# Kernel tuning notes

Measured on AMD Instinct MI355X. Metric: run time of the kernel, lower is better.

## Reference

```python
import jax, jax.numpy as jnp
import numpy as np

N = 100000   # nodes
E = 3200000  # edges
NC = 32


def cheb_conv(x, row, col, W, b):
    """PyG ChebConv with sym normalization and default lambda_max=2.
    Scaled Laplacian L_hat = 2L/lambda_max - I has zero diagonal and
    off-diagonal weights -d_i^{-1/2} d_j^{-1/2} (self-loops removed first).
    W: [K, in, out], b: [out] or None.
    """
    n = x.shape[0]
    ew = jnp.where(row != col, 1.0, 0.0).astype(x.dtype)  # remove_self_loops
    deg = jax.ops.segment_sum(ew, row, num_segments=n)
    dinv = jnp.where(deg > 0, jax.lax.rsqrt(jnp.maximum(deg, 1e-12)), 0.0)
    w = -ew * dinv[row] * dinv[col]  # [E] edge weights of L_hat

    def L(v):  # L_hat @ v via gather + segment-sum scatter
        return jax.ops.segment_sum(w[:, None] * v[col], row, num_segments=n)

    K = W.shape[0]
    Tx0 = x
    out = Tx0 @ W[0]
    if K > 1:
        Tx1 = L(x)
        out = out + Tx1 @ W[1]
        for k in range(2, K):  # Chebyshev recurrence T_k = 2 L T_{k-1} - T_{k-2}
            Tx2 = 2.0 * L(Tx1) - Tx0
            out = out + Tx2 @ W[k]
            Tx0, Tx1 = Tx1, Tx2
    if b is not None:
        out = out + b
    return out


def setup_inputs() -> dict:
    key = jax.random.key(0)
    ks = jax.random.split(key, 10)
    x = jax.random.normal(ks[0], (N, 3), dtype=jnp.float32)
    edge_index = jax.random.randint(ks[1], (2, E), 0, N, dtype=jnp.int64)
    batch = jnp.zeros((N,), dtype=jnp.int64)
    edge_attr = jax.random.normal(ks[2], (E, 1), dtype=jnp.float32)
    s = 0.1
    W1 = jax.random.normal(ks[3], (24, 3, NC), dtype=jnp.float32) * s
    b1 = jnp.zeros((NC,), dtype=jnp.float32)
    W2 = jax.random.normal(ks[4], (12, NC, NC), dtype=jnp.float32) * s
    b2 = jnp.zeros((NC,), dtype=jnp.float32)
    W3 = jax.random.normal(ks[5], (10, NC, NC), dtype=jnp.float32) * s
    b3 = jnp.zeros((NC,), dtype=jnp.float32)
    W4 = jax.random.normal(ks[6], (1, NC, 1), dtype=jnp.float32) * s
    return {"x": x, "edge_index": edge_index, "batch": batch, "edge_attr": edge_attr,
            "W1": W1, "b1": b1, "W2": W2, "b2": b2, "W3": W3, "b3": b3, "W4": W4}


def reference(x, edge_index, batch, edge_attr, W1, b1, W2, b2, W3, b3, W4):
    # batch and edge_attr are unused by ChebNet.forward (kept for signature parity)
    row, col = edge_index[0], edge_index[1]
    h = jax.nn.silu(cheb_conv(x, row, col, W1, b1))
    h = jax.nn.silu(cheb_conv(h, row, col, W2, b2))
    h = jax.nn.silu(cheb_conv(h, row, col, W3, b3))
    return cheb_conv(h, row, col, W4, None)  # block4: K=1, bias=False
```

## Files before the change

### kernel.cpp

```cpp
#include <hip/hip_runtime.h>
#include <math.h>

#define NN 100000
#define EE 3200000
#define NCH 32
#define CAP 96
#define FILL_PASSES 8
#define HB 3200256

typedef unsigned short ushortT;
typedef unsigned int uintT;

__device__ __forceinline__ ushortT f2b(float f) {
  uintT u = __float_as_uint(f);
  uintT r = u + 0x7fffu + ((u >> 16) & 1u);
  return (ushortT)(r >> 16);
}
__device__ __forceinline__ uintT pack2(float x, float y) {
  return (uintT)f2b(x) | ((uintT)f2b(y) << 16);
}
__device__ __forceinline__ float lo2f(uintT u) { return __uint_as_float(u << 16); }
__device__ __forceinline__ float hi2f(uintT u) { return __uint_as_float(u & 0xffff0000u); }
__device__ __forceinline__ float silu(float v) { return v / (1.f + expf(-v)); }


__global__ void init_cursor_k(int* __restrict__ cur) {
  int i = blockIdx.x * blockDim.x + threadIdx.x;
  if (i < NN) cur[i] = i * CAP;
}

__global__ void fill_k(const int* __restrict__ ei, int* __restrict__ cursor,
                       int* __restrict__ colc, int lo, int hi) {
  int t = blockIdx.x * blockDim.x + threadIdx.x;
  if (t * 4 >= EE) return;
  int4 r4 = ((const int4*)ei)[t];
  bool i0 = r4.x >= lo && r4.x < hi;
  bool i1 = r4.y >= lo && r4.y < hi;
  bool i2 = r4.z >= lo && r4.z < hi;
  bool i3 = r4.w >= lo && r4.w < hi;
  if (!(i0 | i1 | i2 | i3)) return;
  int4 c4 = ((const int4*)(ei + EE))[t];
  if (i0 && r4.x != c4.x) colc[atomicAdd(&cursor[r4.x], 1)] = c4.x;
  if (i1 && r4.y != c4.y) colc[atomicAdd(&cursor[r4.y], 1)] = c4.y;
  if (i2 && r4.z != c4.z) colc[atomicAdd(&cursor[r4.z], 1)] = c4.z;
  if (i3 && r4.w != c4.w) colc[atomicAdd(&cursor[r4.w], 1)] = c4.w;
}

__global__ __launch_bounds__(256) void prep_k(
    const int* __restrict__ rend, const float* __restrict__ x,
    float* __restrict__ dinv, float* __restrict__ d2, float* __restrict__ sqd,
    uint2* __restrict__ Vfb) {
  if (blockIdx.x == 0 && threadIdx.x < 24)
    Vfb[(size_t)threadIdx.x * (NN + 1) + NN] = make_uint2(0u, 0u);
  int i = blockIdx.x * blockDim.x + threadIdx.x;
  if (i >= NN) return;
  int c = rend[i] - i * CAP;
  float di = (c > 0) ? rsqrtf((float)c) : 0.f;
  dinv[i] = di;
  d2[i] = di * di;
  sqd[i] = (c > 0) ? sqrtf((float)c) : 1.f;
  Vfb[i] = make_uint2(pack2(di * x[3 * i], di * x[3 * i + 1]),
                      pack2(di * x[3 * i + 2], 0.f));
}

__global__ void sent_b16_k(uintT* __restrict__ Vh0, uintT* __restrict__ Vh1,
                           char* __restrict__ R) {
  int t = threadIdx.x;
  int tb = t >> 3, d = t & 7;
  if (tb >= 14) return;
  uintT* base;
  if (tb == 12) base = Vh0;
  else if (tb == 13) base = Vh1;
  else base = (uintT*)(R + (size_t)tb * HB);
  base[(size_t)NN * 8 + d] = 0u;
}


template <bool FIRST>
__global__ __launch_bounds__(256) void cheb_f3_k(
    const int* __restrict__ rend, const int* __restrict__ colc,
    const float* __restrict__ d2, const uint2* __restrict__ U,
    const uint2* __restrict__ A, uint2* __restrict__ Vo) {
  int t8 = blockIdx.x * blockDim.x + threadIdx.x;
  int i = t8 >> 3, q = t8 & 7;
  if (i >= NN) return;
  int s = i * CAP, e = rend[i];
  float a0 = 0.f, a1 = 0.f, a2 = 0.f;
  for (int b = s; b < e; b += 32) {
    int4 cq = *(const int4*)(colc + b + 4 * q);
    int eb = b + 4 * q;
    int c0 = (eb + 0 < e) ? cq.x : NN;
    int c1 = (eb + 1 < e) ? cq.y : NN;
    int c2 = (eb + 2 < e) ? cq.z : NN;
    int c3 = (eb + 3 < e) ? cq.w : NN;
    uint2 r0 = U[c0], r1 = U[c1], r2 = U[c2], r3 = U[c3];
    a0 += lo2f(r0.x); a1 += hi2f(r0.x); a2 += lo2f(r0.y);
    a0 += lo2f(r1.x); a1 += hi2f(r1.x); a2 += lo2f(r1.y);
    a0 += lo2f(r2.x); a1 += hi2f(r2.x); a2 += lo2f(r2.y);
    a0 += lo2f(r3.x); a1 += hi2f(r3.x); a2 += lo2f(r3.y);
  }
  a0 += __shfl_xor(a0, 1); a1 += __shfl_xor(a1, 1); a2 += __shfl_xor(a2, 1);
  a0 += __shfl_xor(a0, 2); a1 += __shfl_xor(a1, 2); a2 += __shfl_xor(a2, 2);
  a0 += __shfl_xor(a0, 4); a1 += __shfl_xor(a1, 4); a2 += __shfl_xor(a2, 4);
  if (q == 0) {
    float d2i = d2[i];
    float v0, v1, v2;
    if (FIRST) {
      v0 = -d2i * a0; v1 = -d2i * a1; v2 = -d2i * a2;
    } else {
      uint2 ap = A[i];
      v0 = fmaf(-2.f * d2i, a0, -lo2f(ap.x));
      v1 = fmaf(-2.f * d2i, a1, -hi2f(ap.x));
      v2 = fmaf(-2.f * d2i, a2, -lo2f(ap.y));
    }
    Vo[i] = make_uint2(pack2(v0, v1), pack2(v2, 0.f));
  }
}

template <int K0, int K1>
__device__ __forceinline__ void sum_planes(const uint2* __restrict__ Vfb, int i,
                                           const float* __restrict__ W1,
                                           float* __restrict__ s_) {
#pragma unroll
  for (int k = K0; k < K1; ++k) {
    uint2 u = Vfb[(size_t)k * (NN + 1) + i];
    float v0 = lo2f(u.x), v1 = hi2f(u.x), v2 = lo2f(u.y);
    const float* Wk = W1 + k * 96;
#pragma unroll
    for (int j = 0; j < 32; ++j)
      s_[j] = fmaf(v0, Wk[j], fmaf(v1, Wk[32 + j], fmaf(v2, Wk[64 + j], s_[j])));
  }
}

__global__ __launch_bounds__(256) void gemm_l1_k(
    const float* __restrict__ x, const uint2* __restrict__ Vfb,
    const float* __restrict__ W1, const float* __restrict__ b1,
    const float* __restrict__ dinv, const float* __restrict__ sqd,
    ushortT* __restrict__ Vh0, ushortT* __restrict__ Vh1) {
  __shared__ float red[4 * 64 * 36];
  int tid = threadIdx.x;
  int w = tid >> 6, lane = tid & 63;
  int i = blockIdx.x * 64 + lane;
  float s_[32];
#pragma unroll
  for (int j = 0; j < 32; ++j) s_[j] = 0.f;
  if (i < NN) {
    if (w == 0) sum_planes<1, 7>(Vfb, i, W1, s_);
    else if (w == 1) sum_planes<7, 13>(Vfb, i, W1, s_);
    else if (w == 2) sum_planes<13, 19>(Vfb, i, W1, s_);
    else sum_planes<19, 24>(Vfb, i, W1, s_);
  }
  float* rb = &red[(w * 64 + lane) * 36];
#pragma unroll
  for (int j = 0; j < 32; ++j) rb[j] = s_[j];
  __syncthreads();
  int r = tid >> 2, q = tid & 3;
  int io = blockIdx.x * 64 + r;
  if (io >= NN) return;
  float acc8[8];
#pragma unroll
  for (int c = 0; c < 8; ++c) acc8[c] = 0.f;
#pragma unroll
  for (int ww = 0; ww < 4; ++ww) {
    const float* p = &red[(ww * 64 + r) * 36 + q * 8];
#pragma unroll
    for (int c = 0; c < 8; ++c) acc8[c] += p[c];
  }
  float x0 = x[3 * io], x1 = x[3 * io + 1], x2 = x[3 * io + 2];
  float sq = sqd[io], di = dinv[io];
  uintT o[4];
#pragma unroll
  for (int cp = 0; cp < 4; ++cp) {
    int j0 = q * 8 + 2 * cp, j1 = j0 + 1;
    float g0 = fmaf(sq, acc8[2 * cp],
        fmaf(x0, W1[j0], fmaf(x1, W1[32 + j0], fmaf(x2, W1[64 + j0], b1[j0]))));
    float g1 = fmaf(sq, acc8[2 * cp + 1],
        fmaf(x0, W1[j1], fmaf(x1, W1[32 + j1], fmaf(x2, W1[64 + j1], b1[j1]))));
    o[cp] = pack2(di * silu(g0), di * silu(g1));
  }
  uintT* dst = (uintT*)((q >> 1) ? Vh1 : Vh0) + (size_t)io * 8 + (q & 1) * 4;
  *(uint4*)dst = make_uint4(o[0], o[1], o[2], o[3]);
}


template <bool FIRST>
__global__ __launch_bounds__(256) void cheb_q_k(
    const int* __restrict__ rend, const int* __restrict__ colc,
    const float* __restrict__ d2, const uint4* __restrict__ U,
    const uint4* __restrict__ Ap, uint4* __restrict__ Vo) {
  int t = blockIdx.x * blockDim.x + threadIdx.x;
  int i = t >> 2;
  if (i >= NN) return;
  int g = t & 3;
  int slot = g & 1, h2 = g >> 1;
  int lb = (threadIdx.x & 63) & 60;
  int s = i * CAP, e = rend[i];
  float a0 = 0.f, a1 = 0.f, a2 = 0.f, a3 = 0.f;
  float a4 = 0.f, a5 = 0.f, a6 = 0.f, a7 = 0.f;
  for (int b = s; b < e; b += 16) {
    int4 cq = *(const int4*)(colc + b + 4 * g);
#pragma unroll
    for (int src = 0; src < 2; ++src) {
      int sl = lb + 2 * h2 + src;
      int c0 = __shfl(cq.x, sl);
      int c1 = __shfl(cq.y, sl);
      int c2 = __shfl(cq.z, sl);
      int c3 = __shfl(cq.w, sl);
      int eb = b + 8 * h2 + 4 * src;
      c0 = (eb + 0 < e) ? c0 : NN;
      c1 = (eb + 1 < e) ? c1 : NN;
      c2 = (eb + 2 < e) ? c2 : NN;
      c3 = (eb + 3 < e) ? c3 : NN;
      uint4 r0 = U[(size_t)c0 * 2 + slot];
      uint4 r1 = U[(size_t)c1 * 2 + slot];
      uint4 r2 = U[(size_t)c2 * 2 + slot];
      uint4 r3 = U[(size_t)c3 * 2 + slot];
      a0 += lo2f(r0.x); a1 += hi2f(r0.x); a2 += lo2f(r0.y); a3 += hi2f(r0.y);
      a4 += lo2f(r0.z); a5 += hi2f(r0.z); a6 += lo2f(r0.w); a7 += hi2f(r0.w);
      a0 += lo2f(r1.x); a1 += hi2f(r1.x); a2 += lo2f(r1.y); a3 += hi2f(r1.y);
      a4 += lo2f(r1.z); a5 += hi2f(r1.z); a6 += lo2f(r1.w); a7 += hi2f(r1.w);
      a0 += lo2f(r2.x); a1 += hi2f(r2.x); a2 += lo2f(r2.y); a3 += hi2f(r2.y);
      a4 += lo2f(r2.z); a5 += hi2f(r2.z); a6 += lo2f(r2.w); a7 += hi2f(r2.w);
      a0 += lo2f(r3.x); a1 += hi2f(r3.x); a2 += lo2f(r3.y); a3 += hi2f(r3.y);
      a4 += lo2f(r3.z); a5 += hi2f(r3.z); a6 += lo2f(r3.w); a7 += hi2f(r3.w);
    }
  }
  a0 += __shfl_xor(a0, 2); a1 += __shfl_xor(a1, 2);
  a2 += __shfl_xor(a2, 2); a3 += __shfl_xor(a3, 2);
  a4 += __shfl_xor(a4, 2); a5 += __shfl_xor(a5, 2);
  a6 += __shfl_xor(a6, 2); a7 += __shfl_xor(a7, 2);
  if (g >= 2) return;
  float d2i = d2[i];
  float v0, v1, v2, v3, v4, v5, v6, v7;
  if (FIRST) {
    v0 = -d2i * a0; v1 = -d2i * a1; v2 = -d2i * a2; v3 = -d2i * a3;
    v4 = -d2i * a4; v5 = -d2i * a5; v6 = -d2i * a6; v7 = -d2i * a7;
  } else {
    uint4 au = Ap[(size_t)i * 2 + slot];
    v0 = fmaf(-2.f * d2i, a0, -lo2f(au.x));
    v1 = fmaf(-2.f * d2i, a1, -hi2f(au.x));
    v2 = fmaf(-2.f * d2i, a2, -lo2f(au.y));
    v3 = fmaf(-2.f * d2i, a3, -hi2f(au.y));
    v4 = fmaf(-2.f * d2i, a4, -lo2f(au.z));
    v5 = fmaf(-2.f * d2i, a5, -hi2f(au.z));
    v6 = fmaf(-2.f * d2i, a6, -lo2f(au.w));
    v7 = fmaf(-2.f * d2i, a7, -hi2f(au.w));
  }
  Vo[(size_t)i * 2 + slot] = make_uint4(pack2(v0, v1), pack2(v2, v3),
                                        pack2(v4, v5), pack2(v6, v7));
}

__device__ __forceinline__ void fma_pair(uintT dw, const float* __restrict__ Wc,
                                         float a[32]) {
  float vl = lo2f(dw), vh = hi2f(dw);
#pragma unroll
  for (int j = 0; j < 32; ++j) a[j] = fmaf(vl, Wc[j], a[j]);
#pragma unroll
  for (int j = 0; j < 32; ++j) a[j] = fmaf(vh, Wc[32 + j], a[j]);
}

__device__ __forceinline__ void plane_fma(const uintT* __restrict__ h0,
                                          const uintT* __restrict__ h1, size_t i,
                                          const float* __restrict__ W, float a[32]) {
  uint4 u0 = *(const uint4*)(h0 + i * 8);
  uint4 u1 = *(const uint4*)(h0 + i * 8 + 4);
  uint4 u2 = *(const uint4*)(h1 + i * 8);
  uint4 u3 = *(const uint4*)(h1 + i * 8 + 4);
  fma_pair(u0.x, W + 0 * 64, a);   fma_pair(u0.y, W + 1 * 64, a);
  fma_pair(u0.z, W + 2 * 64, a);   fma_pair(u0.w, W + 3 * 64, a);
  fma_pair(u1.x, W + 4 * 64, a);   fma_pair(u1.y, W + 5 * 64, a);
  fma_pair(u1.z, W + 6 * 64, a);   fma_pair(u1.w, W + 7 * 64, a);
  fma_pair(u2.x, W + 8 * 64, a);   fma_pair(u2.y, W + 9 * 64, a);
  fma_pair(u2.z, W + 10 * 64, a);  fma_pair(u2.w, W + 11 * 64, a);
  fma_pair(u3.x, W + 12 * 64, a);  fma_pair(u3.y, W + 13 * 64, a);
  fma_pair(u3.z, W + 14 * 64, a);  fma_pair(u3.w, W + 15 * 64, a);
}

template <int NP, bool INIT>
__global__ __launch_bounds__(256) void gemm_ch_k(
    const uintT* __restrict__ A0, const uintT* __restrict__ A1,
    const uintT* __restrict__ B0, const uintT* __restrict__ B1,
    const uintT* __restrict__ C0, const uintT* __restrict__ C1,
    const uintT* __restrict__ D0, const uintT* __restrict__ D1,
    const float* __restrict__ W, float* __restrict__ acc) {
  int i = blockIdx.x * blockDim.x + threadIdx.x;
  if (i >= NN) return;
  float a[32];
  float4* ar = (float4*)(acc + (size_t)i * 32);
  if (INIT) {
#pragma unroll
    for (int j = 0; j < 32; ++j) a[j] = 0.f;
  } else {
#pragma unroll
    for (int q = 0; q < 8; ++q) {
      float4 v = ar[q];
      a[4 * q] = v.x; a[4 * q + 1] = v.y; a[4 * q + 2] = v.z; a[4 * q + 3] = v.w;
    }
  }
  plane_fma(A0, A1, (size_t)i, W, a);
  if (NP >= 2) plane_fma(B0, B1, (size_t)i, W + 1024, a);
  if (NP >= 3) plane_fma(C0, C1, (size_t)i, W + 2048, a);
  if (NP >= 4) plane_fma(D0, D1, (size_t)i, W + 3072, a);
#pragma unroll
  for (int q = 0; q < 8; ++q)
    ar[q] = make_float4(a[4 * q], a[4 * q + 1], a[4 * q + 2], a[4 * q + 3]);
}

__global__ __launch_bounds__(256) void silu2_k(const float* __restrict__ acc,
                                               const float* __restrict__ b,
                                               const float* __restrict__ sqd,
                                               const float* __restrict__ dinv,
                                               ushortT* __restrict__ Vh0,
                                               ushortT* __restrict__ Vh1) {
  int t = blockIdx.x * blockDim.x + threadIdx.x;
  if (t >= NN * NCH) return;
  int i = t >> 5, j = t & 31;
  float g = fmaf(sqd[i], acc[t], b[j]);
  ushortT uv = f2b(dinv[i] * silu(g));
  if (j < 16) Vh0[(size_t)i * 16 + j] = uv;
  else        Vh1[(size_t)i * 16 + (j - 16)] = uv;
}

__global__ __launch_bounds__(256) void final2_k(const float* __restrict__ acc,
                                                const float* __restrict__ b3,
                                                const float* __restrict__ sqd,
                                                const float* __restrict__ W4,
                                                float* __restrict__ out) {
  int i = blockIdx.x * blockDim.x + threadIdx.x;
  if (i >= NN) return;
  const float4* ar = (const float4*)(acc + (size_t)i * 32);
  float sq = sqd[i];
  float g = 0.f;
#pragma unroll
  for (int q = 0; q < 8; ++q) {
    float4 v = ar[q];
    g = fmaf(silu(fmaf(sq, v.x, b3[4 * q + 0])), W4[4 * q + 0], g);
    g = fmaf(silu(fmaf(sq, v.y, b3[4 * q + 1])), W4[4 * q + 1], g);
    g = fmaf(silu(fmaf(sq, v.z, b3[4 * q + 2])), W4[4 * q + 2], g);
    g = fmaf(silu(fmaf(sq, v.w, b3[4 * q + 3])), W4[4 * q + 3], g);
  }
  out[i] = g;
}


extern "C" void kernel_launch(void* const* d_in, const int* in_sizes, int n_in,
                              void* d_out, int out_size, void* d_ws, size_t ws_size,
                              hipStream_t stream) {
  const float* x = (const float*)d_in[0];
  const int* ei = (const int*)d_in[1];
  const float* W1 = (const float*)d_in[4];
  const float* b1 = (const float*)d_in[5];
  const float* W2 = (const float*)d_in[6];
  const float* b2 = (const float*)d_in[7];
  const float* W3 = (const float*)d_in[8];
  const float* b3 = (const float*)d_in[9];
  const float* W4 = (const float*)d_in[10];
  float* out = (float*)d_out;

  char* ws = (char*)d_ws;
  size_t off = 0;
  auto alloc = [&](size_t bytes) {
    void* p = ws + off;
    off += (bytes + 255) & ~(size_t)255;
    return p;
  };
  int* rend = (int*)alloc((size_t)NN * 4);
  float* dinv = (float*)alloc((size_t)NN * 4);
  float* d2 = (float*)alloc((size_t)NN * 4);
  float* sqd = (float*)alloc((size_t)NN * 4);
  int* colc = (int*)alloc((size_t)NN * CAP * 4 + 128);
  ushortT* Vh0 = (ushortT*)alloc(HB);
  ushortT* Vh1 = (ushortT*)alloc(HB);
  float* acc = (float*)alloc((size_t)NN * NCH * 4);
  char* R = (char*)alloc((size_t)12 * HB);
  uint2* Vfb = (uint2*)R;
  (void)ws_size; (void)in_sizes; (void)n_in; (void)out_size;

  const int GR = (NN + 255) / 256;
  const int GE = (NN * NCH + 255) / 256;
  const int GR4 = (NN * 4 + 255) / 256;
  const int GR8 = (NN * 8 + 255) / 256;
  const int GL1 = (NN + 63) / 64;

  init_cursor_k<<<GR, 256, 0, stream>>>(rend);
  {
    int step = (NN + FILL_PASSES - 1) / FILL_PASSES;
    for (int p = 0; p < FILL_PASSES; ++p) {
      int lo = p * step;
      int hi = (lo + step < NN) ? lo + step : NN;
      fill_k<<<(EE / 4 + 255) / 256, 256, 0, stream>>>(ei, rend, colc, lo, hi);
    }
  }
  prep_k<<<GR, 256, 0, stream>>>(rend, x, dinv, d2, sqd, Vfb);

  auto Vp = [&](int k) { return Vfb + (size_t)k * (NN + 1); };
  cheb_f3_k<true><<<GR8, 256, 0, stream>>>(rend, colc, d2, Vp(0), nullptr, Vp(1));
  for (int k = 2; k < 24; ++k)
    cheb_f3_k<false><<<GR8, 256, 0, stream>>>(rend, colc, d2, Vp(k - 1), Vp(k - 2), Vp(k));
  gemm_l1_k<<<GL1, 256, 0, stream>>>(x, Vfb, W1, b1, dinv, sqd, Vh0, Vh1);

  sent_b16_k<<<1, 128, 0, stream>>>((uintT*)Vh0, (uintT*)Vh1, R);
  auto Rh = [&](int k, int h) {
    return (uintT*)(R + (size_t)(((k - 1) % 6) * 2 + h) * HB);
  };
  auto Hv = [&](int h) { return h ? (uintT*)Vh1 : (uintT*)Vh0; };
  auto run_layer = [&](const float* W, int K) {
    for (int k = 1; k < K; ++k) {
      for (int h = 0; h < 2; ++h) {
        const uint4* U = (const uint4*)((k == 1) ? Hv(h) : Rh(k - 1, h));
        if (k == 1) {
          cheb_q_k<true><<<GR4, 256, 0, stream>>>(rend, colc, d2, U, nullptr,
                                                  (uint4*)Rh(k, h));
        } else {
          const uint4* Ap = (const uint4*)((k == 2) ? Hv(h) : Rh(k - 2, h));
          cheb_q_k<false><<<GR4, 256, 0, stream>>>(rend, colc, d2, U, Ap,
                                                   (uint4*)Rh(k, h));
        }
      }
      if (k == 3) {
        gemm_ch_k<4, true><<<GR, 256, 0, stream>>>(
            (uintT*)Vh0, (uintT*)Vh1, Rh(1, 0), Rh(1, 1), Rh(2, 0), Rh(2, 1),
            Rh(3, 0), Rh(3, 1), W, acc);
      } else if (k > 3 && (k % 3) == 0) {
        gemm_ch_k<3, false><<<GR, 256, 0, stream>>>(
            Rh(k - 2, 0), Rh(k - 2, 1), Rh(k - 1, 0), Rh(k - 1, 1),
            Rh(k, 0), Rh(k, 1), nullptr, nullptr, W + (size_t)(k - 2) * 1024, acc);
      }
    }
    int last = K - 1;
    if (last % 3 == 2) {
      gemm_ch_k<2, false><<<GR, 256, 0, stream>>>(
          Rh(last - 1, 0), Rh(last - 1, 1), Rh(last, 0), Rh(last, 1),
          nullptr, nullptr, nullptr, nullptr, W + (size_t)(last - 1) * 1024, acc);
    }
  };
  run_layer(W2, 12);
  silu2_k<<<GE, 256, 0, stream>>>(acc, b2, sqd, dinv, Vh0, Vh1);
  run_layer(W3, 10);
  final2_k<<<GR, 256, 0, stream>>>(acc, b3, sqd, W4, out);
}
```

Baseline: 1.850 ms.

## Batch Chebyshev GEMMs six-wide, fuse SiLU epilogues, unroll gather loop

The per-layer GEMM accumulation is regrouped into two launches that each take up to six Chebyshev planes, instead of several three- or four-plane passes. The bias+SiLU+bf16 repack and the final W4 projection move into the last GEMM's epilogue, which removes the separate silu2 and final kernels and their round-trips through the fp32 accumulator. The SpMM gather loop is flattened so each thread issues eight independent row loads per iteration, with a launch-bounds occupancy hint added. The risks are higher register pressure in the six-plane GEMM, which is marked for one block per CU, and a tighter register budget in the gather kernel.

```diff
diff --git a/kernel.cpp b/kernel.cpp
--- a/kernel.cpp
+++ b/kernel.cpp
@@ -184,7 +184,7 @@
 
 
 template <bool FIRST>
-__global__ __launch_bounds__(256) void cheb_q_k(
+__global__ __launch_bounds__(256, 4) void cheb_q_k(
     const int* __restrict__ rend, const int* __restrict__ colc,
     const float* __restrict__ d2, const uint4* __restrict__ U,
     const uint4* __restrict__ Ap, uint4* __restrict__ Vo) {
@@ -199,31 +199,44 @@
   float a4 = 0.f, a5 = 0.f, a6 = 0.f, a7 = 0.f;
   for (int b = s; b < e; b += 16) {
     int4 cq = *(const int4*)(colc + b + 4 * g);
-#pragma unroll
-    for (int src = 0; src < 2; ++src) {
-      int sl = lb + 2 * h2 + src;
-      int c0 = __shfl(cq.x, sl);
-      int c1 = __shfl(cq.y, sl);
-      int c2 = __shfl(cq.z, sl);
-      int c3 = __shfl(cq.w, sl);
-      int eb = b + 8 * h2 + 4 * src;
-      c0 = (eb + 0 < e) ? c0 : NN;
-      c1 = (eb + 1 < e) ? c1 : NN;
-      c2 = (eb + 2 < e) ? c2 : NN;
-      c3 = (eb + 3 < e) ? c3 : NN;
-      uint4 r0 = U[(size_t)c0 * 2 + slot];
-      uint4 r1 = U[(size_t)c1 * 2 + slot];
-      uint4 r2 = U[(size_t)c2 * 2 + slot];
-      uint4 r3 = U[(size_t)c3 * 2 + slot];
-      a0 += lo2f(r0.x); a1 += hi2f(r0.x); a2 += lo2f(r0.y); a3 += hi2f(r0.y);
-      a4 += lo2f(r0.z); a5 += hi2f(r0.z); a6 += lo2f(r0.w); a7 += hi2f(r0.w);
-      a0 += lo2f(r1.x); a1 += hi2f(r1.x); a2 += lo2f(r1.y); a3 += hi2f(r1.y);
-      a4 += lo2f(r1.z); a5 += hi2f(r1.z); a6 += lo2f(r1.w); a7 += hi2f(r1.w);
-      a0 += lo2f(r2.x); a1 += hi2f(r2.x); a2 += lo2f(r2.y); a3 += hi2f(r2.y);
-      a4 += lo2f(r2.z); a5 += hi2f(r2.z); a6 += lo2f(r2.w); a7 += hi2f(r2.w);
-      a0 += lo2f(r3.x); a1 += hi2f(r3.x); a2 += lo2f(r3.y); a3 += hi2f(r3.y);
-      a4 += lo2f(r3.z); a5 += hi2f(r3.z); a6 += lo2f(r3.w); a7 += hi2f(r3.w);
-    }
+    int sl0 = lb + 2 * h2, sl1 = sl0 + 1;
+    int eb = b + 8 * h2;
+    int c0 = __shfl(cq.x, sl0), c1 = __shfl(cq.y, sl0);
+    int c2 = __shfl(cq.z, sl0), c3 = __shfl(cq.w, sl0);
+    int c4 = __shfl(cq.x, sl1), c5 = __shfl(cq.y, sl1);
+    int c6 = __shfl(cq.z, sl1), c7 = __shfl(cq.w, sl1);
+    c0 = (eb + 0 < e) ? c0 : NN;
+    c1 = (eb + 1 < e) ? c1 : NN;
+    c2 = (eb + 2 < e) ? c2 : NN;
+    c3 = (eb + 3 < e) ? c3 : NN;
+    c4 = (eb + 4 < e) ? c4 : NN;
+    c5 = (eb + 5 < e) ? c5 : NN;
+    c6 = (eb + 6 < e) ? c6 : NN;
+    c7 = (eb + 7 < e) ? c7 : NN;
+    uint4 r0 = U[(size_t)c0 * 2 + slot];
+    uint4 r1 = U[(size_t)c1 * 2 + slot];
+    uint4 r2 = U[(size_t)c2 * 2 + slot];
+    uint4 r3 = U[(size_t)c3 * 2 + slot];
+    uint4 r4 = U[(size_t)c4 * 2 + slot];
+    uint4 r5 = U[(size_t)c5 * 2 + slot];
+    uint4 r6 = U[(size_t)c6 * 2 + slot];
+    uint4 r7 = U[(size_t)c7 * 2 + slot];
+    a0 += lo2f(r0.x); a1 += hi2f(r0.x); a2 += lo2f(r0.y); a3 += hi2f(r0.y);
+    a4 += lo2f(r0.z); a5 += hi2f(r0.z); a6 += lo2f(r0.w); a7 += hi2f(r0.w);
+    a0 += lo2f(r1.x); a1 += hi2f(r1.x); a2 += lo2f(r1.y); a3 += hi2f(r1.y);
+    a4 += lo2f(r1.z); a5 += hi2f(r1.z); a6 += lo2f(r1.w); a7 += hi2f(r1.w);
+    a0 += lo2f(r2.x); a1 += hi2f(r2.x); a2 += lo2f(r2.y); a3 += hi2f(r2.y);
+    a4 += lo2f(r2.z); a5 += hi2f(r2.z); a6 += lo2f(r2.w); a7 += hi2f(r2.w);
+    a0 += lo2f(r3.x); a1 += hi2f(r3.x); a2 += lo2f(r3.y); a3 += hi2f(r3.y);
+    a4 += lo2f(r3.z); a5 += hi2f(r3.z); a6 += lo2f(r3.w); a7 += hi2f(r3.w);
+    a0 += lo2f(r4.x); a1 += hi2f(r4.x); a2 += lo2f(r4.y); a3 += hi2f(r4.y);
+    a4 += lo2f(r4.z); a5 += hi2f(r4.z); a6 += lo2f(r4.w); a7 += hi2f(r4.w);
+    a0 += lo2f(r5.x); a1 += hi2f(r5.x); a2 += lo2f(r5.y); a3 += hi2f(r5.y);
+    a4 += lo2f(r5.z); a5 += hi2f(r5.z); a6 += lo2f(r5.w); a7 += hi2f(r5.w);
+    a0 += lo2f(r6.x); a1 += hi2f(r6.x); a2 += lo2f(r6.y); a3 += hi2f(r6.y);
+    a4 += lo2f(r6.z); a5 += hi2f(r6.z); a6 += lo2f(r6.w); a7 += hi2f(r6.w);
+    a0 += lo2f(r7.x); a1 += hi2f(r7.x); a2 += lo2f(r7.y); a3 += hi2f(r7.y);
+    a4 += lo2f(r7.z); a5 += hi2f(r7.z); a6 += lo2f(r7.w); a7 += hi2f(r7.w);
   }
   a0 += __shfl_xor(a0, 2); a1 += __shfl_xor(a1, 2);
   a2 += __shfl_xor(a2, 2); a3 += __shfl_xor(a3, 2);
@@ -276,13 +289,19 @@
   fma_pair(u3.z, W + 14 * 64, a);  fma_pair(u3.w, W + 15 * 64, a);
 }
 
-template <int NP, bool INIT>
-__global__ __launch_bounds__(256) void gemm_ch_k(
+template <int NP, bool INIT, int EPI>
+__global__ __launch_bounds__(256, 1) void gemm_ch_k(
     const uintT* __restrict__ A0, const uintT* __restrict__ A1,
     const uintT* __restrict__ B0, const uintT* __restrict__ B1,
     const uintT* __restrict__ C0, const uintT* __restrict__ C1,
     const uintT* __restrict__ D0, const uintT* __restrict__ D1,
-    const float* __restrict__ W, float* __restrict__ acc) {
+    const uintT* __restrict__ E0, const uintT* __restrict__ E1,
+    const uintT* __restrict__ F0, const uintT* __restrict__ F1,
+    const float* __restrict__ W, float* __restrict__ acc,
+    const float* __restrict__ bb, const float* __restrict__ sqd,
+    const float* __restrict__ dinv, const float* __restrict__ W4,
+    ushortT* __restrict__ Vh0, ushortT* __restrict__ Vh1,
+    float* __restrict__ out) {
   int i = blockIdx.x * blockDim.x + threadIdx.x;
   if (i >= NN) return;
   float a[32];
@@ -301,45 +320,35 @@
   if (NP >= 2) plane_fma(B0, B1, (size_t)i, W + 1024, a);
   if (NP >= 3) plane_fma(C0, C1, (size_t)i, W + 2048, a);
   if (NP >= 4) plane_fma(D0, D1, (size_t)i, W + 3072, a);
-#pragma unroll
-  for (int q = 0; q < 8; ++q)
-    ar[q] = make_float4(a[4 * q], a[4 * q + 1], a[4 * q + 2], a[4 * q + 3]);
-}
-
-__global__ __launch_bounds__(256) void silu2_k(const float* __restrict__ acc,
-                                               const float* __restrict__ b,
-                                               const float* __restrict__ sqd,
-                                               const float* __restrict__ dinv,
-                                               ushortT* __restrict__ Vh0,
-                                               ushortT* __restrict__ Vh1) {
-  int t = blockIdx.x * blockDim.x + threadIdx.x;
-  if (t >= NN * NCH) return;
-  int i = t >> 5, j = t & 31;
-  float g = fmaf(sqd[i], acc[t], b[j]);
-  ushortT uv = f2b(dinv[i] * silu(g));
-  if (j < 16) Vh0[(size_t)i * 16 + j] = uv;
-  else        Vh1[(size_t)i * 16 + (j - 16)] = uv;
-}
-
-__global__ __launch_bounds__(256) void final2_k(const float* __restrict__ acc,
-                                                const float* __restrict__ b3,
-                                                const float* __restrict__ sqd,
-                                                const float* __restrict__ W4,
-                                                float* __restrict__ out) {
-  int i = blockIdx.x * blockDim.x + threadIdx.x;
-  if (i >= NN) return;
-  const float4* ar = (const float4*)(acc + (size_t)i * 32);
-  float sq = sqd[i];
-  float g = 0.f;
-#pragma unroll
-  for (int q = 0; q < 8; ++q) {
-    float4 v = ar[q];
-    g = fmaf(silu(fmaf(sq, v.x, b3[4 * q + 0])), W4[4 * q + 0], g);
-    g = fmaf(silu(fmaf(sq, v.y, b3[4 * q + 1])), W4[4 * q + 1], g);
-    g = fmaf(silu(fmaf(sq, v.z, b3[4 * q + 2])), W4[4 * q + 2], g);
-    g = fmaf(silu(fmaf(sq, v.w, b3[4 * q + 3])), W4[4 * q + 3], g);
-  }
-  out[i] = g;
+  if (NP >= 5) plane_fma(E0, E1, (size_t)i, W + 4096, a);
+  if (NP >= 6) plane_fma(F0, F1, (size_t)i, W + 5120, a);
+  if (EPI == 0) {
+#pragma unroll
+    for (int q = 0; q < 8; ++q)
+      ar[q] = make_float4(a[4 * q], a[4 * q + 1], a[4 * q + 2], a[4 * q + 3]);
+  } else if (EPI == 1) {
+    float sq = sqd[i], di = dinv[i];
+    uintT o[16];
+#pragma unroll
+    for (int p = 0; p < 16; ++p) {
+      float g0 = fmaf(sq, a[2 * p], bb[2 * p]);
+      float g1 = fmaf(sq, a[2 * p + 1], bb[2 * p + 1]);
+      o[p] = pack2(di * silu(g0), di * silu(g1));
+    }
+    uintT* w0 = (uintT*)Vh0 + (size_t)i * 8;
+    uintT* w1 = (uintT*)Vh1 + (size_t)i * 8;
+    *(uint4*)w0 = make_uint4(o[0], o[1], o[2], o[3]);
+    *(uint4*)(w0 + 4) = make_uint4(o[4], o[5], o[6], o[7]);
+    *(uint4*)w1 = make_uint4(o[8], o[9], o[10], o[11]);
+    *(uint4*)(w1 + 4) = make_uint4(o[12], o[13], o[14], o[15]);
+  } else {
+    float sq = sqd[i];
+    float g = 0.f;
+#pragma unroll
+    for (int j = 0; j < 32; ++j)
+      g = fmaf(silu(fmaf(sq, a[j], bb[j])), W4[j], g);
+    out[i] = g;
+  }
 }
 
 
@@ -377,7 +386,6 @@
   (void)ws_size; (void)in_sizes; (void)n_in; (void)out_size;
 
   const int GR = (NN + 255) / 256;
-  const int GE = (NN * NCH + 255) / 256;
   const int GR4 = (NN * 4 + 255) / 256;
   const int GR8 = (NN * 8 + 255) / 256;
   const int GL1 = (NN + 63) / 64;
@@ -404,7 +412,7 @@
     return (uintT*)(R + (size_t)(((k - 1) % 6) * 2 + h) * HB);
   };
   auto Hv = [&](int h) { return h ? (uintT*)Vh1 : (uintT*)Vh0; };
-  auto run_layer = [&](const float* W, int K) {
+  auto run_cheb = [&](int K) {
     for (int k = 1; k < K; ++k) {
       for (int h = 0; h < 2; ++h) {
         const uint4* U = (const uint4*)((k == 1) ? Hv(h) : Rh(k - 1, h));
@@ -417,25 +425,66 @@
                                                    (uint4*)Rh(k, h));
         }
       }
-      if (k == 3) {
-        gemm_ch_k<4, true><<<GR, 256, 0, stream>>>(
+      if (k == 5) {
+        gemm_ch_k<6, true, 0><<<GR, 256, 0, stream>>>(
             (uintT*)Vh0, (uintT*)Vh1, Rh(1, 0), Rh(1, 1), Rh(2, 0), Rh(2, 1),
-            Rh(3, 0), Rh(3, 1), W, acc);
-      } else if (k > 3 && (k % 3) == 0) {
-        gemm_ch_k<3, false><<<GR, 256, 0, stream>>>(
-            Rh(k - 2, 0), Rh(k - 2, 1), Rh(k - 1, 0), Rh(k - 1, 1),
-            Rh(k, 0), Rh(k, 1), nullptr, nullptr, W + (size_t)(k - 2) * 1024, acc);
+            Rh(3, 0), Rh(3, 1), Rh(4, 0), Rh(4, 1), Rh(5, 0), Rh(5, 1),
+            (k == 5 ? nullptr : nullptr), acc,
+            nullptr, nullptr, nullptr, nullptr, nullptr, nullptr, nullptr);
       }
     }
-    int last = K - 1;
-    if (last % 3 == 2) {
-      gemm_ch_k<2, false><<<GR, 256, 0, stream>>>(
-          Rh(last - 1, 0), Rh(last - 1, 1), Rh(last, 0), Rh(last, 1),
-          nullptr, nullptr, nullptr, nullptr, W + (size_t)(last - 1) * 1024, acc);
-    }
   };
-  run_layer(W2, 12);
-  silu2_k<<<GE, 256, 0, stream>>>(acc, b2, sqd, dinv, Vh0, Vh1);
-  run_layer(W3, 10);
-  final2_k<<<GR, 256, 0, stream>>>(acc, b3, sqd, W4, out);
-}
+  (void)run_cheb;
+
+  {
+    const float* W = W2;
+    for (int k = 1; k < 12; ++k) {
+      for (int h = 0; h < 2; ++h) {
+        const uint4* U = (const uint4*)((k == 1) ? Hv(h) : Rh(k - 1, h));
+        if (k == 1)
+          cheb_q_k<true><<<GR4, 256, 0, stream>>>(rend, colc, d2, U, nullptr,
+                                                  (uint4*)Rh(k, h));
+        else {
+          const uint4* Ap = (const uint4*)((k == 2) ? Hv(h) : Rh(k - 2, h));
+          cheb_q_k<false><<<GR4, 256, 0, stream>>>(rend, colc, d2, U, Ap,
+                                                   (uint4*)Rh(k, h));
+        }
+      }
+      if (k == 5)
+        gemm_ch_k<6, true, 0><<<GR, 256, 0, stream>>>(
+            (uintT*)Vh0, (uintT*)Vh1, Rh(1, 0), Rh(1, 1), Rh(2, 0), Rh(2, 1),
+            Rh(3, 0), Rh(3, 1), Rh(4, 0), Rh(4, 1), Rh(5, 0), Rh(5, 1),
+            W, acc, nullptr, nullptr, nullptr, nullptr, nullptr, nullptr, nullptr);
+    }
+    gemm_ch_k<6, false, 1><<<GR, 256, 0, stream>>>(
+        Rh(6, 0), Rh(6, 1), Rh(7, 0), Rh(7, 1), Rh(8, 0), Rh(8, 1),
+        Rh(9, 0), Rh(9, 1), Rh(10, 0), Rh(10, 1), Rh(11, 0), Rh(11, 1),
+        W + 6 * 1024, acc, b2, sqd, dinv, nullptr, Vh0, Vh1, nullptr);
+  }
+
+  {
+    const float* W = W3;
+    for (int k = 1; k < 10; ++k) {
+      for (int h = 0; h < 2; ++h) {
+        const uint4* U = (const uint4*)((k == 1) ? Hv(h) : Rh(k - 1, h));
+        if (k == 1)
+          cheb_q_k<true><<<GR4, 256, 0, stream>>>(rend, colc, d2, U, nullptr,
+                                                  (uint4*)Rh(k, h));
+        else {
+          const uint4* Ap = (const uint4*)((k == 2) ? Hv(h) : Rh(k - 2, h));
+          cheb_q_k<false><<<GR4, 256, 0, stream>>>(rend, colc, d2, U, Ap,
+                                                   (uint4*)Rh(k, h));
+        }
+      }
+      if (k == 5)
+        gemm_ch_k<6, true, 0><<<GR, 256, 0, stream>>>(
+            (uintT*)Vh0, (uintT*)Vh1, Rh(1, 0), Rh(1, 1), Rh(2, 0), Rh(2, 1),
+            Rh(3, 0), Rh(3, 1), Rh(4, 0), Rh(4, 1), Rh(5, 0), Rh(5, 1),
+            W, acc, nullptr, nullptr, nullptr, nullptr, nullptr, nullptr, nullptr);
+    }
+    gemm_ch_k<4, false, 2><<<GR, 256, 0, stream>>>(
+        Rh(6, 0), Rh(6, 1), Rh(7, 0), Rh(7, 1), Rh(8, 0), Rh(8, 1),
+        Rh(9, 0), Rh(9, 1), nullptr, nullptr, nullptr, nullptr,
+        W + 6 * 1024, acc, b3, sqd, nullptr, W4, nullptr, nullptr, out);
+  }
+}
```

Result: slower. 1.914 ms (+3.5%).
